# Performance work log

Measured on AMD Instinct MI355X. Metric: run time of the kernel, lower is better.

## Reference

```python
import jax, jax.numpy as jnp
import numpy as np

B, N, D, D_A, S, D_K = 512, 8192, 1024, 512, 8, 64

def setup_inputs() -> dict:
    key = jax.random.key(0)
    k1, k2, k3, k4 = jax.random.split(key, 4)
    lecun_q = 1.0 / np.sqrt(D_A)
    lecun_k = 1.0 / np.sqrt(D)
    return {
        "z": jax.random.normal(k1, (B, D_A), dtype=jnp.float32),
        "pool_vectors": jax.random.normal(k2, (N, D), dtype=jnp.float32),
        "W_Q": jax.random.normal(k3, (S, D_A, D_K), dtype=jnp.float32) * lecun_q,
        "W_K": jax.random.normal(k4, (S, D, D_K), dtype=jnp.float32) * lecun_k,
        "aspect_logits": jnp.zeros((S,), dtype=jnp.float32),
        "tau": jnp.asarray(0.5, dtype=jnp.float32),
        "lambda_sharp": jnp.asarray(10.0, dtype=jnp.float32),
        "temperature": jnp.asarray(0.1, dtype=jnp.float32),
    }

def reference(z, pool_vectors, W_Q, W_K, aspect_logits, tau, lambda_sharp, temperature):
    # Per-aspect projections
    queries = jnp.einsum('bd,adq->baq', z, W_Q)              # [B, S, d_k]
    keys = jnp.einsum('np,apq->naq', pool_vectors, W_K)       # [N, S, d_k]
    # L2 normalize along d_k
    q_norm = queries / (jnp.linalg.norm(queries, axis=-1, keepdims=True) + 1e-08)
    k_norm = keys / (jnp.linalg.norm(keys, axis=-1, keepdims=True) + 1e-08)
    # Multi-aspect cosine similarity
    sims = jnp.einsum('baq,naq->bna', q_norm, k_norm)          # [B, N, S]
    # Learned aspect weighting
    w = jax.nn.softmax(aspect_logits)                          # [S]
    scores = jnp.einsum('bna,a->bn', sims, w)                  # [B, N]
    # Sigmoid gate against threshold, temperature-scaled normalize
    g = jax.nn.sigmoid(lambda_sharp * (scores - tau))
    alpha_raw = g * jnp.exp(scores / temperature)
    alpha = alpha_raw / (jnp.sum(alpha_raw, axis=-1, keepdims=True) + 1e-08)
    return (alpha, scores, keys)
```

## Files before the change

### kernel.cpp

```cpp
#include <hip/hip_runtime.h>
#include <stdint.h>

#define B_DIM 512
#define N_DIM 8192
#define D_DIM 1024
#define DA_DIM 512
#define S_DIM 8
#define DK_DIM 64
#define C_DIM 512

typedef short v8s __attribute__((ext_vector_type(8)));
typedef float v4f __attribute__((ext_vector_type(4)));

__device__ __forceinline__ unsigned int f2bf(float x) {
    union { float f; unsigned int u; } v; v.f = x;
    unsigned int u = v.u;
    return (u + 0x7fffu + ((u >> 16) & 1u)) >> 16;
}

__device__ __forceinline__ void gld16(const unsigned short* g, unsigned short* l) {
    __builtin_amdgcn_global_load_lds(
        (const __attribute__((address_space(1))) unsigned int*)g,
        (__attribute__((address_space(3))) unsigned int*)l,
        16, 0, 0);
}

__device__ __forceinline__ void cvt8(const float* __restrict__ src,
                                     unsigned short* __restrict__ dst, int t) {
    const float4* s4 = (const float4*)src;
    float4 a = s4[2 * t], b = s4[2 * t + 1];
    uint4 o;
    o.x = f2bf(a.x) | (f2bf(a.y) << 16);
    o.y = f2bf(a.z) | (f2bf(a.w) << 16);
    o.z = f2bf(b.x) | (f2bf(b.y) << 16);
    o.w = f2bf(b.z) | (f2bf(b.w) << 16);
    ((uint4*)dst)[t] = o;
}

__device__ __forceinline__ void w_transpose_tile(const float* __restrict__ w,
                                                 unsigned short* __restrict__ wt,
                                                 int a, int dt, int ddim,
                                                 unsigned short* T ) {
    int t = threadIdx.x;
    int d0 = dt * 64;
    int kc4 = (t & 15) * 4;
    const float4* src = (const float4*)(w + ((size_t)a * ddim + d0) * DK_DIM);
    #pragma unroll
    for (int p = 0; p < 4; p++) {
        int dr = p * 16 + (t >> 4);
        float4 v = src[dr * 16 + (t & 15)];
        uint2 pk;
        pk.x = f2bf(v.x) | (f2bf(v.y) << 16);
        pk.y = f2bf(v.z) | (f2bf(v.w) << 16);
        *(uint2*)&T[dr * 68 + kc4] = pk;
    }
    __syncthreads();
    int c0 = a * 64;
    #pragma unroll
    for (int q = 0; q < 2; q++) {
        int k = q * 32 + (t >> 3);
        int ch = t & 7;
        unsigned short s[8];
        #pragma unroll
        for (int i = 0; i < 8; i++) s[i] = T[(ch * 8 + i) * 68 + k];
        uint4 o;
        o.x = (unsigned)s[0] | ((unsigned)s[1] << 16);
        o.y = (unsigned)s[2] | ((unsigned)s[3] << 16);
        o.z = (unsigned)s[4] | ((unsigned)s[5] << 16);
        o.w = (unsigned)s[6] | ((unsigned)s[7] << 16);
        *(uint4*)&wt[(size_t)(c0 + k) * ddim + d0 + ch * 8] = o;
    }
}

__global__ __launch_bounds__(256) void prep(const float* __restrict__ pool,
                                            const float* __restrict__ z,
                                            const float* __restrict__ W_Q,
                                            const float* __restrict__ W_K,
                                            unsigned short* __restrict__ poolb,
                                            unsigned short* __restrict__ zb,
                                            unsigned short* __restrict__ wqt,
                                            unsigned short* __restrict__ wtb) {
    __shared__ unsigned short T[64 * 68];
    int blk = blockIdx.x;
    if (blk < 4096) {
        cvt8(pool, poolb, blk * 256 + threadIdx.x);
    } else if (blk < 4224) {
        cvt8(z, zb, (blk - 4096) * 256 + threadIdx.x);
    } else if (blk < 4352) {
        int idx = blk - 4224;
        w_transpose_tile(W_K, wtb, idx >> 4, idx & 15, D_DIM, T);
    } else {
        int idx = blk - 4352;
        w_transpose_tile(W_Q, wqt, idx >> 3, idx & 7, DA_DIM, T);
    }
}

__device__ __forceinline__ void gemm_mainloop(const unsigned short* __restrict__ A, int lda,
                                              const unsigned short* __restrict__ Bm, int ldb,
                                              int mbase, int nbase, int kiters,
                                              unsigned short (*As)[4096],
                                              unsigned short (*Bs)[4096],
                                              v4f acc[4][4]) {
    int tid = threadIdx.x;
    int wid = tid >> 6, lane = tid & 63;
    int wm = wid >> 1, wn = wid & 1;
    int quad = lane >> 4, l16 = lane & 15;
    int srow = lane >> 2;
    int scol = (lane & 3) * 8;

    auto stage = [&](int kk, int p) {
        #pragma unroll
        for (int j = 0; j < 2; j++) {
            int rgrp = wid * 2 + j;
            int row = rgrp * 16 + srow;
            gld16(&A[(size_t)(mbase + row) * lda + kk * 32 + scol], &As[p][rgrp * 512]);
            gld16(&Bm[(size_t)(nbase + row) * ldb + kk * 32 + scol], &Bs[p][rgrp * 512]);
        }
    };

    stage(0, 0);
    for (int kk = 0; kk < kiters; kk++) {
        __syncthreads();
        if (kk + 1 < kiters) stage(kk + 1, (kk + 1) & 1);
        int p = kk & 1;
        v8s af[4], bf[4];
        #pragma unroll
        for (int mt = 0; mt < 4; mt++)
            af[mt] = *(const v8s*)&As[p][(wm * 64 + mt * 16 + l16) * 32 + quad * 8];
        #pragma unroll
        for (int nt = 0; nt < 4; nt++)
            bf[nt] = *(const v8s*)&Bs[p][(wn * 64 + nt * 16 + l16) * 32 + quad * 8];
        #pragma unroll
        for (int mt = 0; mt < 4; mt++)
            #pragma unroll
            for (int nt = 0; nt < 4; nt++)
                acc[mt][nt] = __builtin_amdgcn_mfma_f32_16x16x32_bf16(
                    af[mt], bf[nt], acc[mt][nt], 0, 0, 0);
    }
}

__global__ __launch_bounds__(256) void fused_gemms(const unsigned short* __restrict__ poolb,
                                                   const unsigned short* __restrict__ wtb,
                                                   const unsigned short* __restrict__ zb,
                                                   const unsigned short* __restrict__ wqt,
                                                   const float* __restrict__ logits,
                                                   float* __restrict__ keys_out,
                                                   unsigned short* __restrict__ kb,
                                                   unsigned short* __restrict__ qwb) {
    __shared__ unsigned short As[2][4096], Bs[2][4096];
    v4f acc[4][4];
    #pragma unroll
    for (int mt = 0; mt < 4; mt++)
        #pragma unroll
        for (int nt = 0; nt < 4; nt++) acc[mt][nt] = (v4f)(0.f);

    int blk = blockIdx.x;
    bool is_q = blk >= 256;
    const unsigned short* A;
    const unsigned short* Bm;
    int lda, mbase, nbase, kiters;
    if (is_q) {
        int q = blk - 256;
        A = zb; Bm = wqt; lda = DA_DIM; kiters = DA_DIM / 32;
        mbase = (q >> 2) * 128; nbase = (q & 3) * 128;
    } else {
        A = poolb; Bm = wtb; lda = D_DIM; kiters = D_DIM / 32;
        mbase = (blk >> 2) * 128; nbase = (blk & 3) * 128;
    }

    gemm_mainloop(A, lda, Bm, lda, mbase, nbase, kiters, As, Bs, acc);

    int tid = threadIdx.x, wid = tid >> 6, lane = tid & 63;
    int wm = wid >> 1, wn = wid & 1, quad = lane >> 4, l16 = lane & 15;

    if (is_q) {
        float l[8]; float mx = -1e30f;
        #pragma unroll
        for (int i = 0; i < 8; i++) { l[i] = logits[i]; mx = fmaxf(mx, l[i]); }
        float se = 0.f;
        #pragma unroll
        for (int i = 0; i < 8; i++) { l[i] = __expf(l[i] - mx); se += l[i]; }
        float wa = l[(nbase >> 6) + wn] / se;

        #pragma unroll
        for (int mt = 0; mt < 4; mt++)
            #pragma unroll
            for (int r = 0; r < 4; r++) {
                float ss = 0.f;
                #pragma unroll
                for (int nt = 0; nt < 4; nt++) ss += acc[mt][nt][r] * acc[mt][nt][r];
                ss += __shfl_xor(ss, 1, 64);
                ss += __shfl_xor(ss, 2, 64);
                ss += __shfl_xor(ss, 4, 64);
                ss += __shfl_xor(ss, 8, 64);
                float sc = wa / (sqrtf(ss) + 1e-8f);
                int row = mbase + wm * 64 + mt * 16 + quad * 4 + r;
                #pragma unroll
                for (int nt = 0; nt < 4; nt++) {
                    int col = nbase + wn * 64 + nt * 16 + l16;
                    qwb[(size_t)row * C_DIM + col] =
                        (unsigned short)f2bf(acc[mt][nt][r] * sc);
                }
            }
    } else {
        #pragma unroll
        for (int mt = 0; mt < 4; mt++)
            #pragma unroll
            for (int r = 0; r < 4; r++) {
                float ss = 0.f;
                #pragma unroll
                for (int nt = 0; nt < 4; nt++) ss += acc[mt][nt][r] * acc[mt][nt][r];
                ss += __shfl_xor(ss, 1, 64);
                ss += __shfl_xor(ss, 2, 64);
                ss += __shfl_xor(ss, 4, 64);
                ss += __shfl_xor(ss, 8, 64);
                float sc = 1.0f / (sqrtf(ss) + 1e-8f);
                int row = mbase + wm * 64 + mt * 16 + quad * 4 + r;
                #pragma unroll
                for (int nt = 0; nt < 4; nt++) {
                    int col = nbase + wn * 64 + nt * 16 + l16;
                    float s = acc[mt][nt][r];
                    keys_out[(size_t)row * C_DIM + col] = s;
                    kb[(size_t)row * C_DIM + col] = (unsigned short)f2bf(s * sc);
                }
            }
    }
}

__global__ __launch_bounds__(256) void scores_gemm(const unsigned short* __restrict__ qwb,
                                                   const unsigned short* __restrict__ kb,
                                                   float* __restrict__ scores_out,
                                                   float* __restrict__ partials,
                                                   const float* __restrict__ lam_p,
                                                   const float* __restrict__ tau_p,
                                                   const float* __restrict__ temp_p) {
    __shared__ unsigned short As[2][4096], Bs[2][4096];
    __shared__ float rowpart[128];
    v4f acc[4][4];
    #pragma unroll
    for (int mt = 0; mt < 4; mt++)
        #pragma unroll
        for (int nt = 0; nt < 4; nt++) acc[mt][nt] = (v4f)(0.f);

    int mbase = blockIdx.y * 128, nbase = blockIdx.x * 128;
    gemm_mainloop(qwb, C_DIM, kb, C_DIM, mbase, nbase, C_DIM / 32, As, Bs, acc);

    int tid = threadIdx.x, wid = tid >> 6, lane = tid & 63;
    int wm = wid >> 1, wn = wid & 1, quad = lane >> 4, l16 = lane & 15;

    if (tid < 128) rowpart[tid] = 0.f;
    __syncthreads();

    float lam = lam_p[0], tau = tau_p[0], invT = 1.0f / temp_p[0];
    float rsum[4][4];
    #pragma unroll
    for (int mt = 0; mt < 4; mt++)
        #pragma unroll
        for (int r = 0; r < 4; r++) rsum[mt][r] = 0.f;

    #pragma unroll
    for (int mt = 0; mt < 4; mt++)
        #pragma unroll
        for (int nt = 0; nt < 4; nt++)
            #pragma unroll
            for (int r = 0; r < 4; r++) {
                float s = acc[mt][nt][r];
                int row = mbase + wm * 64 + mt * 16 + quad * 4 + r;
                int col = nbase + wn * 64 + nt * 16 + l16;
                scores_out[(size_t)row * N_DIM + col] = s;
                float g = 1.0f / (1.0f + __expf(-lam * (s - tau)));
                rsum[mt][r] += g * __expf(s * invT);
            }
    #pragma unroll
    for (int mt = 0; mt < 4; mt++)
        #pragma unroll
        for (int r = 0; r < 4; r++) {
            float v = rsum[mt][r];
            v += __shfl_xor(v, 1, 64);
            v += __shfl_xor(v, 2, 64);
            v += __shfl_xor(v, 4, 64);
            v += __shfl_xor(v, 8, 64);
            if (l16 == 0)
                atomicAdd(&rowpart[wm * 64 + mt * 16 + quad * 4 + r], v);
        }
    __syncthreads();
    if (tid < 128)
        partials[(size_t)blockIdx.x * B_DIM + mbase + tid] = rowpart[tid];
}

__global__ __launch_bounds__(256) void alpha_kernel(const float* __restrict__ scores,
                                                    const float* __restrict__ partials,
                                                    float* __restrict__ alpha,
                                                    const float* __restrict__ lam_p,
                                                    const float* __restrict__ tau_p,
                                                    const float* __restrict__ temp_p) {
    __shared__ float s_inv;
    int b = blockIdx.x;
    int tid = threadIdx.x;
    if (tid < 64) {
        float v = partials[(size_t)tid * B_DIM + b];
        v += __shfl_xor(v, 1, 64);
        v += __shfl_xor(v, 2, 64);
        v += __shfl_xor(v, 4, 64);
        v += __shfl_xor(v, 8, 64);
        v += __shfl_xor(v, 16, 64);
        v += __shfl_xor(v, 32, 64);
        if (tid == 0) s_inv = 1.0f / (v + 1e-8f);
    }
    __syncthreads();
    float inv = s_inv;
    float lam = lam_p[0], tau = tau_p[0], invT = 1.0f / temp_p[0];
    const float4* srow = (const float4*)(scores + (size_t)b * N_DIM);
    float4* arow = (float4*)(alpha + (size_t)b * N_DIM);
    #pragma unroll
    for (int i = 0; i < 8; i++) {
        int idx = tid + i * 256;
        float4 s4 = srow[idx];
        float4 o;
        o.x = (1.0f / (1.0f + __expf(-lam * (s4.x - tau)))) * __expf(s4.x * invT) * inv;
        o.y = (1.0f / (1.0f + __expf(-lam * (s4.y - tau)))) * __expf(s4.y * invT) * inv;
        o.z = (1.0f / (1.0f + __expf(-lam * (s4.z - tau)))) * __expf(s4.z * invT) * inv;
        o.w = (1.0f / (1.0f + __expf(-lam * (s4.w - tau)))) * __expf(s4.w * invT) * inv;
        arow[idx] = o;
    }
}

extern "C" void kernel_launch(void* const* d_in, const int* in_sizes, int n_in,
                              void* d_out, int out_size, void* d_ws, size_t ws_size,
                              hipStream_t stream) {
    const float* z      = (const float*)d_in[0];
    const float* pool   = (const float*)d_in[1];
    const float* W_Q    = (const float*)d_in[2];
    const float* W_K    = (const float*)d_in[3];
    const float* logits = (const float*)d_in[4];
    const float* tau    = (const float*)d_in[5];
    const float* lam    = (const float*)d_in[6];
    const float* temp   = (const float*)d_in[7];

    float* alpha  = (float*)d_out;
    float* scores = alpha + (size_t)B_DIM * N_DIM;
    float* keys   = scores + (size_t)B_DIM * N_DIM;

    char* ws = (char*)d_ws;
    unsigned short* poolb = (unsigned short*)(ws);
    unsigned short* kb    = (unsigned short*)(ws + 16777216);
    unsigned short* wtb   = (unsigned short*)(ws + 25165824);
    unsigned short* wqt   = (unsigned short*)(ws + 26214400);
    unsigned short* zb    = (unsigned short*)(ws + 26738688);
    unsigned short* qwb   = (unsigned short*)(ws + 27262976);
    float* partials       = (float*)(ws + 27787264);

    prep<<<dim3(4416), dim3(256), 0, stream>>>(pool, z, W_Q, W_K,
                                               poolb, zb, wqt, wtb);
    fused_gemms<<<dim3(272), dim3(256), 0, stream>>>(poolb, wtb, zb, wqt, logits,
                                                     keys, kb, qwb);
    scores_gemm<<<dim3(64, 4), dim3(256), 0, stream>>>(qwb, kb, scores, partials,
                                                       lam, tau, temp);
    alpha_kernel<<<dim3(512), dim3(256), 0, stream>>>(scores, partials, alpha,
                                                      lam, tau, temp);
}
```

Baseline: 157.9 us.

## Replace LDS-staged GEMM mainloop with direct global-to-register MFMA operand loads

Result: slower. 183.2 us (+16.0%).

```diff
diff --git a/kernel.cpp b/kernel.cpp
--- a/kernel.cpp
+++ b/kernel.cpp
@@ -16,13 +16,6 @@
     union { float f; unsigned int u; } v; v.f = x;
     unsigned int u = v.u;
     return (u + 0x7fffu + ((u >> 16) & 1u)) >> 16;
-}
-
-__device__ __forceinline__ void gld16(const unsigned short* g, unsigned short* l) {
-    __builtin_amdgcn_global_load_lds(
-        (const __attribute__((address_space(1))) unsigned int*)g,
-        (__attribute__((address_space(3))) unsigned int*)l,
-        16, 0, 0);
 }
 
 __device__ __forceinline__ void cvt8(const float* __restrict__ src,
@@ -95,41 +88,26 @@
     }
 }
 
-__device__ __forceinline__ void gemm_mainloop(const unsigned short* __restrict__ A, int lda,
-                                              const unsigned short* __restrict__ Bm, int ldb,
-                                              int mbase, int nbase, int kiters,
-                                              unsigned short (*As)[4096],
-                                              unsigned short (*Bs)[4096],
-                                              v4f acc[4][4]) {
+template <int KITERS>
+__device__ __forceinline__ void gemm_reg(const unsigned short* __restrict__ A, int lda,
+                                         const unsigned short* __restrict__ Bm, int ldb,
+                                         int mbase, int nbase, v4f acc[4][4]) {
     int tid = threadIdx.x;
     int wid = tid >> 6, lane = tid & 63;
     int wm = wid >> 1, wn = wid & 1;
     int quad = lane >> 4, l16 = lane & 15;
-    int srow = lane >> 2;
-    int scol = (lane & 3) * 8;
-
-    auto stage = [&](int kk, int p) {
-        #pragma unroll
-        for (int j = 0; j < 2; j++) {
-            int rgrp = wid * 2 + j;
-            int row = rgrp * 16 + srow;
-            gld16(&A[(size_t)(mbase + row) * lda + kk * 32 + scol], &As[p][rgrp * 512]);
-            gld16(&Bm[(size_t)(nbase + row) * ldb + kk * 32 + scol], &Bs[p][rgrp * 512]);
-        }
-    };
-
-    stage(0, 0);
-    for (int kk = 0; kk < kiters; kk++) {
-        __syncthreads();
-        if (kk + 1 < kiters) stage(kk + 1, (kk + 1) & 1);
-        int p = kk & 1;
+    const unsigned short* Ab = A + (size_t)(mbase + wm * 64 + l16) * lda + quad * 8;
+    const unsigned short* Bb = Bm + (size_t)(nbase + wn * 64 + l16) * ldb + quad * 8;
+
+    #pragma unroll
+    for (int kk = 0; kk < KITERS; kk++) {
         v8s af[4], bf[4];
         #pragma unroll
         for (int mt = 0; mt < 4; mt++)
-            af[mt] = *(const v8s*)&As[p][(wm * 64 + mt * 16 + l16) * 32 + quad * 8];
+            af[mt] = *(const v8s*)(Ab + (size_t)mt * 16 * lda + kk * 32);
         #pragma unroll
         for (int nt = 0; nt < 4; nt++)
-            bf[nt] = *(const v8s*)&Bs[p][(wn * 64 + nt * 16 + l16) * 32 + quad * 8];
+            bf[nt] = *(const v8s*)(Bb + (size_t)nt * 16 * ldb + kk * 32);
         #pragma unroll
         for (int mt = 0; mt < 4; mt++)
             #pragma unroll
@@ -139,15 +117,14 @@
     }
 }
 
-__global__ __launch_bounds__(256) void fused_gemms(const unsigned short* __restrict__ poolb,
-                                                   const unsigned short* __restrict__ wtb,
-                                                   const unsigned short* __restrict__ zb,
-                                                   const unsigned short* __restrict__ wqt,
-                                                   const float* __restrict__ logits,
-                                                   float* __restrict__ keys_out,
-                                                   unsigned short* __restrict__ kb,
-                                                   unsigned short* __restrict__ qwb) {
-    __shared__ unsigned short As[2][4096], Bs[2][4096];
+__global__ __launch_bounds__(256, 1) void fused_gemms(const unsigned short* __restrict__ poolb,
+                                                      const unsigned short* __restrict__ wtb,
+                                                      const unsigned short* __restrict__ zb,
+                                                      const unsigned short* __restrict__ wqt,
+                                                      const float* __restrict__ logits,
+                                                      float* __restrict__ keys_out,
+                                                      unsigned short* __restrict__ kb,
+                                                      unsigned short* __restrict__ qwb) {
     v4f acc[4][4];
     #pragma unroll
     for (int mt = 0; mt < 4; mt++)
@@ -156,19 +133,16 @@
 
     int blk = blockIdx.x;
     bool is_q = blk >= 256;
-    const unsigned short* A;
-    const unsigned short* Bm;
-    int lda, mbase, nbase, kiters;
+    int mbase, nbase;
+
     if (is_q) {
         int q = blk - 256;
-        A = zb; Bm = wqt; lda = DA_DIM; kiters = DA_DIM / 32;
         mbase = (q >> 2) * 128; nbase = (q & 3) * 128;
+        gemm_reg<DA_DIM / 32>(zb, DA_DIM, wqt, DA_DIM, mbase, nbase, acc);
     } else {
-        A = poolb; Bm = wtb; lda = D_DIM; kiters = D_DIM / 32;
         mbase = (blk >> 2) * 128; nbase = (blk & 3) * 128;
-    }
-
-    gemm_mainloop(A, lda, Bm, lda, mbase, nbase, kiters, As, Bs, acc);
+        gemm_reg<D_DIM / 32>(poolb, D_DIM, wtb, D_DIM, mbase, nbase, acc);
+    }
 
     int tid = threadIdx.x, wid = tid >> 6, lane = tid & 63;
     int wm = wid >> 1, wn = wid & 1, quad = lane >> 4, l16 = lane & 15;
@@ -227,14 +201,13 @@
     }
 }
 
-__global__ __launch_bounds__(256) void scores_gemm(const unsigned short* __restrict__ qwb,
-                                                   const unsigned short* __restrict__ kb,
-                                                   float* __restrict__ scores_out,
-                                                   float* __restrict__ partials,
-                                                   const float* __restrict__ lam_p,
-                                                   const float* __restrict__ tau_p,
-                                                   const float* __restrict__ temp_p) {
-    __shared__ unsigned short As[2][4096], Bs[2][4096];
+__global__ __launch_bounds__(256, 1) void scores_gemm(const unsigned short* __restrict__ qwb,
+                                                      const unsigned short* __restrict__ kb,
+                                                      float* __restrict__ scores_out,
+                                                      float* __restrict__ partials,
+                                                      const float* __restrict__ lam_p,
+                                                      const float* __restrict__ tau_p,
+                                                      const float* __restrict__ temp_p) {
     __shared__ float rowpart[128];
     v4f acc[4][4];
     #pragma unroll
@@ -243,7 +216,7 @@
         for (int nt = 0; nt < 4; nt++) acc[mt][nt] = (v4f)(0.f);
 
     int mbase = blockIdx.y * 128, nbase = blockIdx.x * 128;
-    gemm_mainloop(qwb, C_DIM, kb, C_DIM, mbase, nbase, C_DIM / 32, As, Bs, acc);
+    gemm_reg<C_DIM / 32>(qwb, C_DIM, kb, C_DIM, mbase, nbase, acc);
 
     int tid = threadIdx.x, wid = tid >> 6, lane = tid & 63;
     int wm = wid >> 1, wn = wid & 1, quad = lane >> 4, l16 = lane & 15;
```

## Halve GEMM tile width to 128x64 so more blocks fill the GPU

Applied to the files above, without the earlier changes.

New measurement: 147.5 us. 1.07x faster.

```diff
diff --git a/kernel.cpp b/kernel.cpp
--- a/kernel.cpp
+++ b/kernel.cpp
@@ -99,22 +99,25 @@
                                               const unsigned short* __restrict__ Bm, int ldb,
                                               int mbase, int nbase, int kiters,
                                               unsigned short (*As)[4096],
-                                              unsigned short (*Bs)[4096],
-                                              v4f acc[4][4]) {
+                                              unsigned short (*Bs)[2048],
+                                              v4f acc[2][4]) {
     int tid = threadIdx.x;
     int wid = tid >> 6, lane = tid & 63;
-    int wm = wid >> 1, wn = wid & 1;
     int quad = lane >> 4, l16 = lane & 15;
     int srow = lane >> 2;
     int scol = (lane & 3) * 8;
 
     auto stage = [&](int kk, int p) {
         #pragma unroll
-        for (int j = 0; j < 2; j++) {
-            int rgrp = wid * 2 + j;
-            int row = rgrp * 16 + srow;
-            gld16(&A[(size_t)(mbase + row) * lda + kk * 32 + scol], &As[p][rgrp * 512]);
-            gld16(&Bm[(size_t)(nbase + row) * ldb + kk * 32 + scol], &Bs[p][rgrp * 512]);
+        for (int j = 0; j < 3; j++) {
+            int g = wid * 3 + j;
+            if (g < 8) {
+                int row = g * 16 + srow;
+                gld16(&A[(size_t)(mbase + row) * lda + kk * 32 + scol], &As[p][g * 512]);
+            } else {
+                int row = (g - 8) * 16 + srow;
+                gld16(&Bm[(size_t)(nbase + row) * ldb + kk * 32 + scol], &Bs[p][(g - 8) * 512]);
+            }
         }
     };
 
@@ -123,15 +126,15 @@
         __syncthreads();
         if (kk + 1 < kiters) stage(kk + 1, (kk + 1) & 1);
         int p = kk & 1;
-        v8s af[4], bf[4];
-        #pragma unroll
-        for (int mt = 0; mt < 4; mt++)
-            af[mt] = *(const v8s*)&As[p][(wm * 64 + mt * 16 + l16) * 32 + quad * 8];
+        v8s af[2], bf[4];
+        #pragma unroll
+        for (int mt = 0; mt < 2; mt++)
+            af[mt] = *(const v8s*)&As[p][(wid * 32 + mt * 16 + l16) * 32 + quad * 8];
         #pragma unroll
         for (int nt = 0; nt < 4; nt++)
-            bf[nt] = *(const v8s*)&Bs[p][(wn * 64 + nt * 16 + l16) * 32 + quad * 8];
-        #pragma unroll
-        for (int mt = 0; mt < 4; mt++)
+            bf[nt] = *(const v8s*)&Bs[p][(nt * 16 + l16) * 32 + quad * 8];
+        #pragma unroll
+        for (int mt = 0; mt < 2; mt++)
             #pragma unroll
             for (int nt = 0; nt < 4; nt++)
                 acc[mt][nt] = __builtin_amdgcn_mfma_f32_16x16x32_bf16(
@@ -139,39 +142,36 @@
     }
 }
 
-__global__ __launch_bounds__(256) void fused_gemms(const unsigned short* __restrict__ poolb,
-                                                   const unsigned short* __restrict__ wtb,
-                                                   const unsigned short* __restrict__ zb,
-                                                   const unsigned short* __restrict__ wqt,
-                                                   const float* __restrict__ logits,
-                                                   float* __restrict__ keys_out,
-                                                   unsigned short* __restrict__ kb,
-                                                   unsigned short* __restrict__ qwb) {
-    __shared__ unsigned short As[2][4096], Bs[2][4096];
-    v4f acc[4][4];
-    #pragma unroll
-    for (int mt = 0; mt < 4; mt++)
+__global__ __launch_bounds__(256, 2) void fused_gemms(const unsigned short* __restrict__ poolb,
+                                                      const unsigned short* __restrict__ wtb,
+                                                      const unsigned short* __restrict__ zb,
+                                                      const unsigned short* __restrict__ wqt,
+                                                      const float* __restrict__ logits,
+                                                      float* __restrict__ keys_out,
+                                                      unsigned short* __restrict__ kb,
+                                                      unsigned short* __restrict__ qwb) {
+    __shared__ unsigned short As[2][4096];
+    __shared__ unsigned short Bs[2][2048];
+    v4f acc[2][4];
+    #pragma unroll
+    for (int mt = 0; mt < 2; mt++)
         #pragma unroll
         for (int nt = 0; nt < 4; nt++) acc[mt][nt] = (v4f)(0.f);
 
     int blk = blockIdx.x;
-    bool is_q = blk >= 256;
-    const unsigned short* A;
-    const unsigned short* Bm;
-    int lda, mbase, nbase, kiters;
+    bool is_q = blk >= 512;
+    int mbase, nbase;
     if (is_q) {
-        int q = blk - 256;
-        A = zb; Bm = wqt; lda = DA_DIM; kiters = DA_DIM / 32;
-        mbase = (q >> 2) * 128; nbase = (q & 3) * 128;
+        int q = blk - 512;
+        mbase = (q >> 3) * 128; nbase = (q & 7) * 64;
+        gemm_mainloop(zb, DA_DIM, wqt, DA_DIM, mbase, nbase, DA_DIM / 32, As, Bs, acc);
     } else {
-        A = poolb; Bm = wtb; lda = D_DIM; kiters = D_DIM / 32;
-        mbase = (blk >> 2) * 128; nbase = (blk & 3) * 128;
-    }
-
-    gemm_mainloop(A, lda, Bm, lda, mbase, nbase, kiters, As, Bs, acc);
+        mbase = (blk >> 3) * 128; nbase = (blk & 7) * 64;
+        gemm_mainloop(poolb, D_DIM, wtb, D_DIM, mbase, nbase, D_DIM / 32, As, Bs, acc);
+    }
 
     int tid = threadIdx.x, wid = tid >> 6, lane = tid & 63;
-    int wm = wid >> 1, wn = wid & 1, quad = lane >> 4, l16 = lane & 15;
+    int quad = lane >> 4, l16 = lane & 15;
 
     if (is_q) {
         float l[8]; float mx = -1e30f;
@@ -180,10 +180,10 @@
         float se = 0.f;
         #pragma unroll
         for (int i = 0; i < 8; i++) { l[i] = __expf(l[i] - mx); se += l[i]; }
-        float wa = l[(nbase >> 6) + wn] / se;
-
-        #pragma unroll
-        for (int mt = 0; mt < 4; mt++)
+        float wa = l[nbase >> 6] / se;
+
+        #pragma unroll
+        for (int mt = 0; mt < 2; mt++)
             #pragma unroll
             for (int r = 0; r < 4; r++) {
                 float ss = 0.f;
@@ -194,17 +194,17 @@
                 ss += __shfl_xor(ss, 4, 64);
                 ss += __shfl_xor(ss, 8, 64);
                 float sc = wa / (sqrtf(ss) + 1e-8f);
-                int row = mbase + wm * 64 + mt * 16 + quad * 4 + r;
+                int row = mbase + wid * 32 + mt * 16 + quad * 4 + r;
                 #pragma unroll
                 for (int nt = 0; nt < 4; nt++) {
-                    int col = nbase + wn * 64 + nt * 16 + l16;
+                    int col = nbase + nt * 16 + l16;
                     qwb[(size_t)row * C_DIM + col] =
                         (unsigned short)f2bf(acc[mt][nt][r] * sc);
                 }
             }
     } else {
         #pragma unroll
-        for (int mt = 0; mt < 4; mt++)
+        for (int mt = 0; mt < 2; mt++)
             #pragma unroll
             for (int r = 0; r < 4; r++) {
                 float ss = 0.f;
@@ -215,10 +215,10 @@
                 ss += __shfl_xor(ss, 4, 64);
                 ss += __shfl_xor(ss, 8, 64);
                 float sc = 1.0f / (sqrtf(ss) + 1e-8f);
-                int row = mbase + wm * 64 + mt * 16 + quad * 4 + r;
+                int row = mbase + wid * 32 + mt * 16 + quad * 4 + r;
                 #pragma unroll
                 for (int nt = 0; nt < 4; nt++) {
-                    int col = nbase + wn * 64 + nt * 16 + l16;
+                    int col = nbase + nt * 16 + l16;
                     float s = acc[mt][nt][r];
                     keys_out[(size_t)row * C_DIM + col] = s;
                     kb[(size_t)row * C_DIM + col] = (unsigned short)f2bf(s * sc);
@@ -227,61 +227,50 @@
     }
 }
 
-__global__ __launch_bounds__(256) void scores_gemm(const unsigned short* __restrict__ qwb,
-                                                   const unsigned short* __restrict__ kb,
-                                                   float* __restrict__ scores_out,
-                                                   float* __restrict__ partials,
-                                                   const float* __restrict__ lam_p,
-                                                   const float* __restrict__ tau_p,
-                                                   const float* __restrict__ temp_p) {
-    __shared__ unsigned short As[2][4096], Bs[2][4096];
+__global__ __launch_bounds__(256, 2) void scores_gemm(const unsigned short* __restrict__ qwb,
+                                                      const unsigned short* __restrict__ kb,
+                                                      float* __restrict__ scores_out,
+                                                      float* __restrict__ partials,
+                                                      const float* __restrict__ lam_p,
+                                                      const float* __restrict__ tau_p,
+                                                      const float* __restrict__ temp_p) {
+    __shared__ unsigned short As[2][4096];
+    __shared__ unsigned short Bs[2][2048];
     __shared__ float rowpart[128];
-    v4f acc[4][4];
-    #pragma unroll
-    for (int mt = 0; mt < 4; mt++)
+    v4f acc[2][4];
+    #pragma unroll
+    for (int mt = 0; mt < 2; mt++)
         #pragma unroll
         for (int nt = 0; nt < 4; nt++) acc[mt][nt] = (v4f)(0.f);
 
-    int mbase = blockIdx.y * 128, nbase = blockIdx.x * 128;
+    int mbase = blockIdx.y * 128, nbase = blockIdx.x * 64;
     gemm_mainloop(qwb, C_DIM, kb, C_DIM, mbase, nbase, C_DIM / 32, As, Bs, acc);
 
     int tid = threadIdx.x, wid = tid >> 6, lane = tid & 63;
-    int wm = wid >> 1, wn = wid & 1, quad = lane >> 4, l16 = lane & 15;
-
-    if (tid < 128) rowpart[tid] = 0.f;
-    __syncthreads();
+    int quad = lane >> 4, l16 = lane & 15;
 
     float lam = lam_p[0], tau = tau_p[0], invT = 1.0f / temp_p[0];
-    float rsum[4][4];
-    #pragma unroll
-    for (int mt = 0; mt < 4; mt++)
-        #pragma unroll
-        for (int r = 0; r < 4; r++) rsum[mt][r] = 0.f;
-
-    #pragma unroll
-    for (int mt = 0; mt < 4; mt++)
-        #pragma unroll
-        for (int nt = 0; nt < 4; nt++)
+
+    #pragma unroll
+    for (int mt = 0; mt < 2; mt++)
+        #pragma unroll
+        for (int r = 0; r < 4; r++) {
+            float rs = 0.f;
+            int row = mbase + wid * 32 + mt * 16 + quad * 4 + r;
             #pragma unroll
-            for (int r = 0; r < 4; r++) {
+            for (int nt = 0; nt < 4; nt++) {
                 float s = acc[mt][nt][r];
-                int row = mbase + wm * 64 + mt * 16 + quad * 4 + r;
-                int col = nbase + wn * 64 + nt * 16 + l16;
+                int col = nbase + nt * 16 + l16;
                 scores_out[(size_t)row * N_DIM + col] = s;
                 float g = 1.0f / (1.0f + __expf(-lam * (s - tau)));
-                rsum[mt][r] += g * __expf(s * invT);
+                rs += g * __expf(s * invT);
             }
-    #pragma unroll
-    for (int mt = 0; mt < 4; mt++)
-        #pragma unroll
-        for (int r = 0; r < 4; r++) {
-            float v = rsum[mt][r];
-            v += __shfl_xor(v, 1, 64);
-            v += __shfl_xor(v, 2, 64);
-            v += __shfl_xor(v, 4, 64);
-            v += __shfl_xor(v, 8, 64);
+            rs += __shfl_xor(rs, 1, 64);
+            rs += __shfl_xor(rs, 2, 64);
+            rs += __shfl_xor(rs, 4, 64);
+            rs += __shfl_xor(rs, 8, 64);
             if (l16 == 0)
-                atomicAdd(&rowpart[wm * 64 + mt * 16 + quad * 4 + r], v);
+                rowpart[wid * 32 + mt * 16 + quad * 4 + r] = rs;
         }
     __syncthreads();
     if (tid < 128)
@@ -294,11 +283,14 @@
                                                     const float* __restrict__ lam_p,
                                                     const float* __restrict__ tau_p,
                                                     const float* __restrict__ temp_p) {
+    __shared__ float red[128];
     __shared__ float s_inv;
     int b = blockIdx.x;
     int tid = threadIdx.x;
+    if (tid < 128) red[tid] = partials[(size_t)tid * B_DIM + b];
+    __syncthreads();
     if (tid < 64) {
-        float v = partials[(size_t)tid * B_DIM + b];
+        float v = red[tid] + red[tid + 64];
         v += __shfl_xor(v, 1, 64);
         v += __shfl_xor(v, 2, 64);
         v += __shfl_xor(v, 4, 64);
@@ -352,10 +344,10 @@
 
     prep<<<dim3(4416), dim3(256), 0, stream>>>(pool, z, W_Q, W_K,
                                                poolb, zb, wqt, wtb);
-    fused_gemms<<<dim3(272), dim3(256), 0, stream>>>(poolb, wtb, zb, wqt, logits,
+    fused_gemms<<<dim3(544), dim3(256), 0, stream>>>(poolb, wtb, zb, wqt, logits,
                                                      keys, kb, qwb);
-    scores_gemm<<<dim3(64, 4), dim3(256), 0, stream>>>(qwb, kb, scores, partials,
-                                                       lam, tau, temp);
+    scores_gemm<<<dim3(128, 4), dim3(256), 0, stream>>>(qwb, kb, scores, partials,
+                                                        lam, tau, temp);
     alpha_kernel<<<dim3(512), dim3(256), 0, stream>>>(scores, partials, alpha,
                                                       lam, tau, temp);
 }
```
